# Kernel tuning notes

Measured on AMD Instinct MI355X. Metric: run time of the kernel, lower is better.

The kernel has to match this reference:

```python
import jax, jax.numpy as jnp
import numpy as np
import math

E = 512
H = 2048
P = 128  # attention_limit

def _make_params(key):
    ks = jax.random.split(key, 6)
    s = 0.02
    p = {}
    p['wq'] = jax.random.normal(ks[0], (E, E), jnp.float32) * s
    p['bq'] = jnp.zeros((E,), jnp.float32)
    p['wk'] = jax.random.normal(ks[1], (E, E), jnp.float32) * s
    p['bk'] = jnp.zeros((E,), jnp.float32)
    p['wv'] = jax.random.normal(ks[2], (E, E), jnp.float32) * s
    p['bv'] = jnp.zeros((E,), jnp.float32)
    p['w1'] = jax.random.normal(ks[3], (E, H), jnp.float32) * s
    p['b1'] = jnp.zeros((H,), jnp.float32)
    p['w2'] = jax.random.normal(ks[4], (H, E), jnp.float32) * s
    p['b2'] = jnp.zeros((E,), jnp.float32)
    p['ln1_w'] = jnp.ones((E,), jnp.float32)
    p['ln1_b'] = jnp.zeros((E,), jnp.float32)
    p['ln2_w'] = jnp.ones((E,), jnp.float32)
    p['ln2_b'] = jnp.zeros((E,), jnp.float32)
    return p

def setup_inputs() -> dict:
    key = jax.random.key(0)
    kx, kp = jax.random.split(key)
    inp = {'x': jax.random.normal(kx, (2, 1024, E), jnp.float32)}
    inp.update(_make_params(kp))
    return inp

def _layernorm(x, w, b, eps=1e-5):
    mu = jnp.mean(x, axis=-1, keepdims=True)
    var = jnp.mean((x - mu) ** 2, axis=-1, keepdims=True)
    return (x - mu) / jnp.sqrt(var + eps) * w + b

def _forward(x, wq, bq, wk, bk, wv, bv, w1, b1, w2, b2, ln1_w, ln1_b, ln2_w, ln2_b):
    B, S, Ed = x.shape
    # "RoPE" is actually additive sinusoidal PE in the source
    pos = jnp.arange(S, dtype=jnp.float32)[:, None]
    div = jnp.exp(jnp.arange(0, Ed, 2, dtype=jnp.float32) * (-math.log(10000.0) / Ed))
    pe = jnp.zeros((S, Ed), jnp.float32)
    pe = pe.at[:, 0::2].set(jnp.sin(pos * div))
    pe = pe.at[:, 1::2].set(jnp.cos(pos * div))
    x = x + pe[None]

    # local attention: pad x first, then apply K/V linears (padded rows -> bias)
    x_ext = jnp.pad(x, ((0, 0), (P, P), (0, 0)))
    q = x @ wq + bq                      # [B,S,E]
    k_ext = x_ext @ wk + bk              # [B,S+2P,E]
    v_ext = x_ext @ wv + bv
    W = 2 * P + 1
    win_idx = jnp.arange(S)[:, None] + jnp.arange(W)[None, :]  # [S,W]
    k_win = k_ext[:, win_idx]            # [B,S,W,E]
    v_win = v_ext[:, win_idx]            # [B,S,W,E]
    energy = jnp.einsum('bse,bswe->bsw', q, k_win) / jnp.sqrt(jnp.float32(Ed))
    attn = jax.nn.softmax(energy, axis=-1)
    attn_out = jnp.einsum('bsw,bswe->bse', attn, v_win)

    x = _layernorm(attn_out + x, ln1_w, ln1_b)
    ff = jnp.maximum(x @ w1 + b1, 0.0) @ w2 + b2
    return _layernorm(ff + x, ln2_w, ln2_b)

def reference(x, wq, bq, wk, bk, wv, bv, w1, b1, w2, b2, ln1_w, ln1_b, ln2_w, ln2_b):
    return _forward(x, wq, bq, wk, bk, wv, bv, w1, b1, w2, b2, ln1_w, ln1_b, ln2_w, ln2_b)
```

## Files before the change

kernel.cpp:

```cpp
#include <hip/hip_runtime.h>
#include <hip/hip_bf16.h>

#define S_LEN 1024
#define E_DIM 512
#define H_DIM 2048
#define EXTA 1296
#define BS_ROWS 2048

typedef __attribute__((ext_vector_type(8))) short bf16x8;
typedef __attribute__((ext_vector_type(4))) float f32x4;

__device__ inline ushort f2bf(float x) {
  union { float f; unsigned u; } c; c.f = x;
  unsigned u = c.u;
  u += 0x7fffu + ((u >> 16) & 1u);
  return (ushort)(u >> 16);
}
__device__ inline float bf2f(ushort u) {
  union { unsigned u; float f; } c;
  c.u = ((unsigned)u) << 16;
  return c.f;
}

__device__ inline void gload16(ushort* dst, const ushort* src) {
  __builtin_amdgcn_global_load_lds(
      (const __attribute__((address_space(1))) void*)src,
      (__attribute__((address_space(3))) void*)dst, 16, 0, 0);
}

__global__ __launch_bounds__(256) void prep_kernel(const float* __restrict__ x,
                                                   const float* __restrict__ wq,
                                                   const float* __restrict__ wk,
                                                   const float* __restrict__ wv,
                                                   ushort* __restrict__ xpe_bf,
                                                   ushort* __restrict__ wqkvT) {
  __shared__ float t[32][33];
  const int blk = blockIdx.x;
  if (blk < 2048) {
    int idx = blk * 256 + threadIdx.x;
    int e = idx & (E_DIM - 1);
    int s = idx >> 9;
    const float c = -9.210340371976184f / 512.0f;
    float freq = expf((float)(e & ~1) * c);
    float ang = (float)s * freq;
    float pe = (e & 1) ? cosf(ang) : sinf(ang);
    xpe_bf[idx] = f2bf(x[idx] + pe);
    xpe_bf[idx + S_LEN * E_DIM] = f2bf(x[idx + S_LEN * E_DIM] + pe);
  } else {
    const int tile = blk - 2048;
    const int sect = tile >> 8, tt = tile & 255;
    const float* W = sect == 0 ? wq : (sect == 1 ? wk : wv);
    ushort* WT = wqkvT + (size_t)sect * 512 * 512;
    const int bx = tt & 15, by = tt >> 4;
    int lx = threadIdx.x & 31, ly = threadIdx.x >> 5;
    int n0 = bx * 32, k0 = by * 32;
#pragma unroll
    for (int r = 0; r < 4; ++r)
      t[ly + r * 8][lx] = W[(size_t)(k0 + ly + r * 8) * 512 + n0 + lx];
    __syncthreads();
#pragma unroll
    for (int r = 0; r < 4; ++r)
      WT[(size_t)(n0 + ly + r * 8) * 512 + k0 + lx] = f2bf(t[lx][ly + r * 8]);
  }
}

__global__ __launch_bounds__(256) void qkv_pad_kernel(const ushort* __restrict__ A,
                                                      const ushort* __restrict__ Bt,
                                                      const float* __restrict__ bq,
                                                      const float* __restrict__ bk,
                                                      const float* __restrict__ bv,
                                                      ushort* __restrict__ q_out,
                                                      ushort* __restrict__ k_out,
                                                      ushort* __restrict__ v_out) {
  __shared__ ushort As[64 * 64];
  __shared__ ushort Bs[128 * 64];
  const int blk = blockIdx.x;
  const int tid = threadIdx.x;

  if (blk >= 384) {
    int p = (blk - 384) * 256 + tid;
    int t2 = p / (2 * 272 * 512);
    int r2 = p % (2 * 272 * 512);
    int b = r2 / (272 * 512);
    int r3 = r2 % (272 * 512);
    if (t2 == 0) {
      int rr = r3 >> 9, e = r3 & 511;
      int row = rr < 128 ? rr : 1024 + rr;
      float v = rr < 256 ? bk[e] : 0.f;
      k_out[((size_t)b * EXTA + row) * 512 + e] = f2bf(v);
    } else {
      int n = r3 / 272, jj = r3 % 272;
      int j = jj < 128 ? jj : 1024 + jj;
      float v = jj < 256 ? bv[n] : 0.f;
      v_out[((size_t)b * 512 + n) * EXTA + j] = f2bf(v);
    }
    return;
  }

  const int lane = tid & 63;
  const int w = tid >> 6;
  const int wr = w >> 1, wc = w & 1;
  const int l15 = lane & 15, lhi = lane >> 4;
  const int col0 = (blk % 12) * 128, row0 = (blk / 12) * 64;

  f32x4 acc[2][4] = {};

  for (int k0 = 0; k0 < 512; k0 += 64) {
#pragma unroll
    for (int it = 0; it < 2; ++it) {
      int u = it * 256 + tid;
      int r = u >> 3;
      int c16 = (u & 7) ^ (r & 7);
      gload16(&As[(size_t)u * 8], &A[(size_t)(row0 + r) * 512 + k0 + c16 * 8]);
    }
#pragma unroll
    for (int it = 0; it < 4; ++it) {
      int u = it * 256 + tid;
      int r = u >> 3;
      int c16 = (u & 7) ^ (r & 7);
      gload16(&Bs[(size_t)u * 8], &Bt[(size_t)(col0 + r) * 512 + k0 + c16 * 8]);
    }
    __syncthreads();
#pragma unroll
    for (int kk = 0; kk < 2; ++kk) {
      bf16x8 af[2], bfr[4];
#pragma unroll
      for (int mi = 0; mi < 2; ++mi) {
        int r = wr * 32 + mi * 16 + l15;
        int c16 = (kk * 4 + lhi) ^ (r & 7);
        af[mi] = *(const bf16x8*)&As[r * 64 + c16 * 8];
      }
#pragma unroll
      for (int ni = 0; ni < 4; ++ni) {
        int r = wc * 64 + ni * 16 + l15;
        int c16 = (kk * 4 + lhi) ^ (r & 7);
        bfr[ni] = *(const bf16x8*)&Bs[r * 64 + c16 * 8];
      }
#pragma unroll
      for (int mi = 0; mi < 2; ++mi)
#pragma unroll
        for (int ni = 0; ni < 4; ++ni)
          acc[mi][ni] = __builtin_amdgcn_mfma_f32_16x16x32_bf16(af[mi], bfr[ni], acc[mi][ni], 0, 0, 0);
    }
    __syncthreads();
  }

#pragma unroll
  for (int mi = 0; mi < 2; ++mi) {
    int mbase = row0 + wr * 32 + mi * 16 + lhi * 4;
#pragma unroll
    for (int ni = 0; ni < 4; ++ni) {
      int n = col0 + wc * 64 + ni * 16 + l15;
      int sect = n >> 9, nn = n & 511;
      float b = sect == 0 ? bq[nn] : (sect == 1 ? bk[nn] : bv[nn]);
      int bb = mbase >> 10;
      int s = mbase & 1023;
      if (sect == 0) {
#pragma unroll
        for (int j = 0; j < 4; ++j)
          q_out[(size_t)(mbase + j) * 512 + nn] = f2bf(acc[mi][ni][j] + b);
      } else if (sect == 1) {
#pragma unroll
        for (int j = 0; j < 4; ++j)
          k_out[((size_t)bb * EXTA + 128 + s + j) * 512 + nn] = f2bf(acc[mi][ni][j] + b);
      } else {
        ushort4 pk;
        pk.x = f2bf(acc[mi][ni][0] + b);
        pk.y = f2bf(acc[mi][ni][1] + b);
        pk.z = f2bf(acc[mi][ni][2] + b);
        pk.w = f2bf(acc[mi][ni][3] + b);
        *(ushort4*)&v_out[((size_t)bb * 512 + nn) * EXTA + 128 + s] = pk;
      }
    }
  }
}

template <int BM, int BN, int WM, int WN, int OUT>
__global__ __launch_bounds__(256) void mfma_gemm(const ushort* __restrict__ A,
                                                 const ushort* __restrict__ Bt,
                                                 const float* __restrict__ bias,
                                                 void* __restrict__ Cout,
                                                 int M, int N, int K, int LDA) {
  constexpr int WAVES_N = BN / WN;
  constexpr int FM = WM / 16, FN = WN / 16;
  __shared__ ushort As[BM * 64];
  __shared__ ushort Bs[BN * 64];
  const int tid = threadIdx.x;
  const int lane = tid & 63;
  const int w = tid >> 6;
  const int wr = w / WAVES_N, wc = w % WAVES_N;
  const int l15 = lane & 15, lhi = lane >> 4;
  const int col0 = blockIdx.x * BN, row0 = blockIdx.y * BM;
  const int koff = blockIdx.z * K;

  f32x4 acc[FM][FN] = {};

  for (int k0 = 0; k0 < K; k0 += 64) {
#pragma unroll
    for (int it = 0; it < BM / 32; ++it) {
      int u = it * 256 + tid;
      int r = u >> 3;
      int c16 = (u & 7) ^ (r & 7);
      gload16(&As[(size_t)u * 8], &A[(size_t)(row0 + r) * LDA + koff + k0 + c16 * 8]);
    }
#pragma unroll
    for (int it = 0; it < BN / 32; ++it) {
      int u = it * 256 + tid;
      int r = u >> 3;
      int c16 = (u & 7) ^ (r & 7);
      gload16(&Bs[(size_t)u * 8], &Bt[(size_t)(col0 + r) * LDA + koff + k0 + c16 * 8]);
    }
    __syncthreads();
#pragma unroll
    for (int kk = 0; kk < 2; ++kk) {
      bf16x8 af[FM], bfr[FN];
#pragma unroll
      for (int mi = 0; mi < FM; ++mi) {
        int r = wr * WM + mi * 16 + l15;
        int c16 = (kk * 4 + lhi) ^ (r & 7);
        af[mi] = *(const bf16x8*)&As[r * 64 + c16 * 8];
      }
#pragma unroll
      for (int ni = 0; ni < FN; ++ni) {
        int r = wc * WN + ni * 16 + l15;
        int c16 = (kk * 4 + lhi) ^ (r & 7);
        bfr[ni] = *(const bf16x8*)&Bs[r * 64 + c16 * 8];
      }
#pragma unroll
      for (int mi = 0; mi < FM; ++mi)
#pragma unroll
        for (int ni = 0; ni < FN; ++ni)
          acc[mi][ni] = __builtin_amdgcn_mfma_f32_16x16x32_bf16(af[mi], bfr[ni], acc[mi][ni], 0, 0, 0);
    }
    __syncthreads();
  }

#pragma unroll
  for (int mi = 0; mi < FM; ++mi) {
    int mbase = row0 + wr * WM + mi * 16 + lhi * 4;
#pragma unroll
    for (int ni = 0; ni < FN; ++ni) {
      int n = col0 + wc * WN + ni * 16 + l15;
      if constexpr (OUT == 1) {
        float b = bias[n];
        ushort* C = (ushort*)Cout;
#pragma unroll
        for (int j = 0; j < 4; ++j)
          C[(size_t)(mbase + j) * N + n] = f2bf(fmaxf(acc[mi][ni][j] + b, 0.f));
      } else {
        float* C = (float*)Cout + (size_t)blockIdx.z * M * N;
#pragma unroll
        for (int j = 0; j < 4; ++j) C[(size_t)(mbase + j) * N + n] = acc[mi][ni][j];
      }
    }
  }
}

union AttnSm {
  struct {
    float e[16][292];
    ushort p[16][296];
    float inv[16];
    float redS[8][16];
    float redQ[8][16];
    float mu[16], rs[16];
  } a;
  float t[32][33];
};

__global__ __launch_bounds__(512) void attn_ln1(const ushort* __restrict__ qb,
                                                const ushort* __restrict__ kb,
                                                const ushort* __restrict__ vt,
                                                const ushort* __restrict__ xpe_bf,
                                                const float* __restrict__ ln1w,
                                                const float* __restrict__ ln1b,
                                                const float* __restrict__ w1,
                                                const float* __restrict__ w2,
                                                ushort* __restrict__ w1T,
                                                ushort* __restrict__ w2T,
                                                ushort* __restrict__ x1bf) {
  __shared__ AttnSm sm;
  const int tid = threadIdx.x;

  if (blockIdx.x >= 128) {
    const int tile = blockIdx.x - 128;
    const float* W; ushort* WT; int K, N, bx, by;
    if (tile < 1024) {
      K = 512; N = 2048; W = w1; WT = w1T;
      bx = tile & 63; by = tile >> 6;
    } else {
      K = 2048; N = 512; W = w2; WT = w2T;
      int tt = tile - 1024; bx = tt & 15; by = tt >> 4;
    }
    int lx = tid & 31, ly = tid >> 5;
    int n0 = bx * 32, k0 = by * 32;
#pragma unroll
    for (int r = 0; r < 2; ++r)
      sm.t[ly + r * 16][lx] = W[(size_t)(k0 + ly + r * 16) * N + n0 + lx];
    __syncthreads();
#pragma unroll
    for (int r = 0; r < 2; ++r)
      WT[(size_t)(n0 + ly + r * 16) * K + k0 + lx] = f2bf(sm.t[lx][ly + r * 16]);
    return;
  }

  const int lane = tid & 63;
  const int w = tid >> 6;
  const int l15 = lane & 15, lhi = lane >> 4;
  const int tile = blockIdx.x;
  const int b = tile >> 6;
  const int s0 = (tile & 63) * 16;
  const int base0 = b * 1024 + s0;

  const ushort* qrow = qb + (size_t)(base0 + l15) * 512 + lhi * 8;
  bf16x8 qf[16];
#pragma unroll
  for (int ks = 0; ks < 16; ++ks) qf[ks] = *(const bf16x8*)(qrow + ks * 32);

  const float scale = 0.044194173824159216f;
  const ushort* kbase = kb + (size_t)b * EXTA * 512 + (size_t)(s0 + l15) * 512 + lhi * 8;

  for (int jt = w; jt < 18; jt += 8) {
    f32x4 acc = {};
    const ushort* kp = kbase + (size_t)jt * 16 * 512;
#pragma unroll
    for (int ks = 0; ks < 16; ++ks) {
      bf16x8 kf = *(const bf16x8*)(kp + ks * 32);
      acc = __builtin_amdgcn_mfma_f32_16x16x32_bf16(qf[ks], kf, acc, 0, 0, 0);
    }
    int jc = jt * 16 + l15;
#pragma unroll
    for (int j = 0; j < 4; ++j) {
      int i = lhi * 4 + j;
      bool valid = (jc >= i) && (jc <= i + 256);
      sm.a.e[i][jc] = valid ? acc[j] * scale : -1e30f;
    }
  }
  __syncthreads();

  {
    int r = tid >> 5, c0 = tid & 31;
    float m = -1e30f;
#pragma unroll
    for (int t = 0; t < 9; ++t) m = fmaxf(m, sm.a.e[r][c0 + 32 * t]);
#pragma unroll
    for (int off = 1; off <= 16; off <<= 1) m = fmaxf(m, __shfl_xor(m, off));
    float s = 0.f;
#pragma unroll
    for (int t = 0; t < 9; ++t) {
      float p = __expf(sm.a.e[r][c0 + 32 * t] - m);
      s += p;
      sm.a.p[r][c0 + 32 * t] = f2bf(p);
    }
#pragma unroll
    for (int off = 1; off <= 16; off <<= 1) s += __shfl_xor(s, off);
    if (c0 == 0) sm.a.inv[r] = 1.0f / s;
  }
  __syncthreads();

  bf16x8 pf[9];
#pragma unroll
  for (int ks = 0; ks < 9; ++ks) pf[ks] = *(const bf16x8*)&sm.a.p[l15][ks * 32 + lhi * 8];
  float inv[4];
#pragma unroll
  for (int j = 0; j < 4; ++j) inv[j] = sm.a.inv[lhi * 4 + j];

  const ushort* vbase = vt + (size_t)b * 512 * EXTA + s0 + lhi * 8;
  float val[4][4];
#pragma unroll
  for (int ni = 0; ni < 4; ++ni) {
    int n = w * 64 + ni * 16 + l15;
    f32x4 acc = {};
    const ushort* vp = vbase + (size_t)n * EXTA;
#pragma unroll
    for (int ks = 0; ks < 9; ++ks) {
      bf16x8 vf = *(const bf16x8*)(vp + ks * 32);
      acc = __builtin_amdgcn_mfma_f32_16x16x32_bf16(pf[ks], vf, acc, 0, 0, 0);
    }
#pragma unroll
    for (int j = 0; j < 4; ++j) {
      int r = lhi * 4 + j;
      val[ni][j] = acc[j] * inv[j] + bf2f(xpe_bf[(size_t)(base0 + r) * 512 + n]);
    }
  }

  float S[4], Q[4];
#pragma unroll
  for (int j = 0; j < 4; ++j) {
    S[j] = 0.f; Q[j] = 0.f;
#pragma unroll
    for (int ni = 0; ni < 4; ++ni) { S[j] += val[ni][j]; Q[j] += val[ni][j] * val[ni][j]; }
  }
#pragma unroll
  for (int off = 1; off <= 8; off <<= 1) {
#pragma unroll
    for (int j = 0; j < 4; ++j) {
      S[j] += __shfl_xor(S[j], off);
      Q[j] += __shfl_xor(Q[j], off);
    }
  }
  if (l15 == 0) {
#pragma unroll
    for (int j = 0; j < 4; ++j) { sm.a.redS[w][lhi * 4 + j] = S[j]; sm.a.redQ[w][lhi * 4 + j] = Q[j]; }
  }
  __syncthreads();
  if (tid < 16) {
    float sS = 0.f, sQ = 0.f;
#pragma unroll
    for (int ww = 0; ww < 8; ++ww) { sS += sm.a.redS[ww][tid]; sQ += sm.a.redQ[ww][tid]; }
    float mu = sS * (1.0f / 512.0f);
    float var = sQ * (1.0f / 512.0f) - mu * mu;
    sm.a.mu[tid] = mu;
    sm.a.rs[tid] = rsqrtf(var + 1e-5f);
  }
  __syncthreads();

#pragma unroll
  for (int ni = 0; ni < 4; ++ni) {
    int n = w * 64 + ni * 16 + l15;
    float lw = ln1w[n], lb = ln1b[n];
#pragma unroll
    for (int j = 0; j < 4; ++j) {
      int r = lhi * 4 + j;
      float o = (val[ni][j] - sm.a.mu[r]) * sm.a.rs[r] * lw + lb;
      x1bf[(size_t)(base0 + r) * 512 + n] = f2bf(o);
    }
  }
}

__device__ inline float wave_reduce_sum(float v) {
#pragma unroll
  for (int off = 32; off >= 1; off >>= 1) v += __shfl_xor(v, off);
  return v;
}

__global__ __launch_bounds__(256) void ln2_kernel(const float* __restrict__ parts,
                                                  const float* __restrict__ ab,
                                                  const ushort* __restrict__ rsd_bf,
                                                  const float* __restrict__ w,
                                                  const float* __restrict__ bias,
                                                  float* __restrict__ out) {
  const int row = blockIdx.x;
  const int tid = threadIdx.x;
  __shared__ float red[8];
  const int e0 = tid * 2;
  const size_t base = (size_t)row * E_DIM + e0;
  const size_t PART = (size_t)BS_ROWS * E_DIM;
  float2 v0 = *(const float2*)(parts + base);
  float2 v1 = *(const float2*)(parts + PART + base);
  float2 bb = *(const float2*)(ab + e0);
  ushort2 rv = *(const ushort2*)(rsd_bf + base);
  float x0 = v0.x + v1.x + bb.x + bf2f(rv.x);
  float x1 = v0.y + v1.y + bb.y + bf2f(rv.y);

  float sm = wave_reduce_sum(x0 + x1);
  if ((tid & 63) == 0) red[tid >> 6] = sm;
  __syncthreads();
  float mu = (red[0] + red[1] + red[2] + red[3]) * (1.0f / 512.0f);
  float d0 = x0 - mu, d1 = x1 - mu;
  float vs = wave_reduce_sum(d0 * d0 + d1 * d1);
  if ((tid & 63) == 0) red[4 + (tid >> 6)] = vs;
  __syncthreads();
  float var = (red[4] + red[5] + red[6] + red[7]) * (1.0f / 512.0f);
  float inv = rsqrtf(var + 1e-5f);
  float2 wv = *(const float2*)(w + e0);
  float2 bi = *(const float2*)(bias + e0);
  float o0 = d0 * inv * wv.x + bi.x;
  float o1 = d1 * inv * wv.y + bi.y;
  *(float2*)(out + base) = make_float2(o0, o1);
}

extern "C" void kernel_launch(void* const* d_in, const int* in_sizes, int n_in,
                              void* d_out, int out_size, void* d_ws, size_t ws_size,
                              hipStream_t stream) {
  const float* x    = (const float*)d_in[0];
  const float* wq   = (const float*)d_in[1];
  const float* bq   = (const float*)d_in[2];
  const float* wk   = (const float*)d_in[3];
  const float* bk   = (const float*)d_in[4];
  const float* wv   = (const float*)d_in[5];
  const float* bv   = (const float*)d_in[6];
  const float* w1   = (const float*)d_in[7];
  const float* b1   = (const float*)d_in[8];
  const float* w2   = (const float*)d_in[9];
  const float* b2   = (const float*)d_in[10];
  const float* ln1w = (const float*)d_in[11];
  const float* ln1b = (const float*)d_in[12];
  const float* ln2w = (const float*)d_in[13];
  const float* ln2b = (const float*)d_in[14];

  char* W = (char*)d_ws;
  ushort* xpebf  = (ushort*)(W);
  ushort* wqkvT  = (ushort*)(W + (2u  << 20));
  ushort* w1T    = (ushort*)(W + (4u  << 20));
  ushort* w2T    = (ushort*)(W + (6u  << 20));
  ushort* q_bf   = (ushort*)(W + (8u  << 20));
  ushort* k_bf   = (ushort*)(W + (10u << 20));
  ushort* v_t    = (ushort*)(W + (13u << 20));
  ushort* x1bf   = (ushort*)(W + (16u << 20));
  ushort* ff1_bf = (ushort*)(W + (18u << 20));
  float*  ff2    = (float*)(W + (26u << 20));

  prep_kernel<<<2816, 256, 0, stream>>>(x, wq, wk, wv, xpebf, wqkvT);

  qkv_pad_kernel<<<2560, 256, 0, stream>>>(xpebf, wqkvT, bq, bk, bv, q_bf, k_bf, v_t);

  attn_ln1<<<2176, 512, 0, stream>>>(q_bf, k_bf, v_t, xpebf, ln1w, ln1b,
                                     w1, w2, w1T, w2T, x1bf);

  mfma_gemm<64, 128, 32, 64, 1><<<dim3(16, 32), 256, 0, stream>>>(
      x1bf, w1T, b1, ff1_bf, BS_ROWS, H_DIM, 512, 512);

  mfma_gemm<64, 64, 32, 32, 3><<<dim3(8, 32, 2), 256, 0, stream>>>(
      ff1_bf, w2T, nullptr, ff2, BS_ROWS, E_DIM, 1024, 2048);

  ln2_kernel<<<BS_ROWS, 256, 0, stream>>>(ff2, b2, x1bf, ln2w, ln2b, (float*)d_out);
}
```

Baseline: 72.39 us.

## Shrink QKV tiles, widen attention blocks to 1024 threads, vectorize PE prep

The positional-encoding prep now handles two adjacent elements per thread, computing one sincos and using float2/ushort2 accesses, which halves that part of the grid. The QKV GEMM tile shrinks from 64x128 to 64x64, doubling the block count so more CUs get work. The attention+LN1 kernel moves to 1024 threads (16 waves), with each wave owning one softmax row and 32 output columns. The trade-offs are less data reuse per QKV tile and higher register and occupancy pressure from the larger attention blocks.

```diff
diff --git a/kernel.cpp b/kernel.cpp
--- a/kernel.cpp
+++ b/kernel.cpp
@@ -36,18 +36,25 @@
                                                    ushort* __restrict__ wqkvT) {
   __shared__ float t[32][33];
   const int blk = blockIdx.x;
-  if (blk < 2048) {
+  if (blk < 1024) {
     int idx = blk * 256 + threadIdx.x;
-    int e = idx & (E_DIM - 1);
-    int s = idx >> 9;
+    int ep = idx & 255;
+    int s = idx >> 8;
+    int e0 = ep * 2;
     const float c = -9.210340371976184f / 512.0f;
-    float freq = expf((float)(e & ~1) * c);
-    float ang = (float)s * freq;
-    float pe = (e & 1) ? cosf(ang) : sinf(ang);
-    xpe_bf[idx] = f2bf(x[idx] + pe);
-    xpe_bf[idx + S_LEN * E_DIM] = f2bf(x[idx + S_LEN * E_DIM] + pe);
+    float freq = __expf((float)e0 * c);
+    float sn, cs;
+    __sincosf((float)s * freq, &sn, &cs);
+    size_t base = (size_t)s * E_DIM + e0;
+    float2 x0 = *(const float2*)(x + base);
+    float2 x1 = *(const float2*)(x + base + S_LEN * E_DIM);
+    ushort2 o0, o1;
+    o0.x = f2bf(x0.x + sn); o0.y = f2bf(x0.y + cs);
+    o1.x = f2bf(x1.x + sn); o1.y = f2bf(x1.y + cs);
+    *(ushort2*)(xpe_bf + base) = o0;
+    *(ushort2*)(xpe_bf + base + S_LEN * E_DIM) = o1;
   } else {
-    const int tile = blk - 2048;
+    const int tile = blk - 1024;
     const int sect = tile >> 8, tt = tile & 255;
     const float* W = sect == 0 ? wq : (sect == 1 ? wk : wv);
     ushort* WT = wqkvT + (size_t)sect * 512 * 512;
@@ -73,12 +80,12 @@
                                                       ushort* __restrict__ k_out,
                                                       ushort* __restrict__ v_out) {
   __shared__ ushort As[64 * 64];
-  __shared__ ushort Bs[128 * 64];
+  __shared__ ushort Bs[64 * 64];
   const int blk = blockIdx.x;
   const int tid = threadIdx.x;
 
-  if (blk >= 384) {
-    int p = (blk - 384) * 256 + tid;
+  if (blk >= 768) {
+    int p = (blk - 768) * 256 + tid;
     int t2 = p / (2 * 272 * 512);
     int r2 = p % (2 * 272 * 512);
     int b = r2 / (272 * 512);
@@ -101,9 +108,9 @@
   const int w = tid >> 6;
   const int wr = w >> 1, wc = w & 1;
   const int l15 = lane & 15, lhi = lane >> 4;
-  const int col0 = (blk % 12) * 128, row0 = (blk / 12) * 64;
-
-  f32x4 acc[2][4] = {};
+  const int col0 = (blk % 24) * 64, row0 = (blk / 24) * 64;
+
+  f32x4 acc[2][2] = {};
 
   for (int k0 = 0; k0 < 512; k0 += 64) {
 #pragma unroll
@@ -114,7 +121,7 @@
       gload16(&As[(size_t)u * 8], &A[(size_t)(row0 + r) * 512 + k0 + c16 * 8]);
     }
 #pragma unroll
-    for (int it = 0; it < 4; ++it) {
+    for (int it = 0; it < 2; ++it) {
       int u = it * 256 + tid;
       int r = u >> 3;
       int c16 = (u & 7) ^ (r & 7);
@@ -123,7 +130,7 @@
     __syncthreads();
 #pragma unroll
     for (int kk = 0; kk < 2; ++kk) {
-      bf16x8 af[2], bfr[4];
+      bf16x8 af[2], bfr[2];
 #pragma unroll
       for (int mi = 0; mi < 2; ++mi) {
         int r = wr * 32 + mi * 16 + l15;
@@ -131,15 +138,15 @@
         af[mi] = *(const bf16x8*)&As[r * 64 + c16 * 8];
       }
 #pragma unroll
-      for (int ni = 0; ni < 4; ++ni) {
-        int r = wc * 64 + ni * 16 + l15;
+      for (int ni = 0; ni < 2; ++ni) {
+        int r = wc * 32 + ni * 16 + l15;
         int c16 = (kk * 4 + lhi) ^ (r & 7);
         bfr[ni] = *(const bf16x8*)&Bs[r * 64 + c16 * 8];
       }
 #pragma unroll
       for (int mi = 0; mi < 2; ++mi)
 #pragma unroll
-        for (int ni = 0; ni < 4; ++ni)
+        for (int ni = 0; ni < 2; ++ni)
           acc[mi][ni] = __builtin_amdgcn_mfma_f32_16x16x32_bf16(af[mi], bfr[ni], acc[mi][ni], 0, 0, 0);
     }
     __syncthreads();
@@ -149,8 +156,8 @@
   for (int mi = 0; mi < 2; ++mi) {
     int mbase = row0 + wr * 32 + mi * 16 + lhi * 4;
 #pragma unroll
-    for (int ni = 0; ni < 4; ++ni) {
-      int n = col0 + wc * 64 + ni * 16 + l15;
+    for (int ni = 0; ni < 2; ++ni) {
+      int n = col0 + wc * 32 + ni * 16 + l15;
       int sect = n >> 9, nn = n & 511;
       float b = sect == 0 ? bq[nn] : (sect == 1 ? bk[nn] : bv[nn]);
       int bb = mbase >> 10;
@@ -261,24 +268,24 @@
     float e[16][292];
     ushort p[16][296];
     float inv[16];
-    float redS[8][16];
-    float redQ[8][16];
+    float redS[16][16];
+    float redQ[16][16];
     float mu[16], rs[16];
   } a;
   float t[32][33];
 };
 
-__global__ __launch_bounds__(512) void attn_ln1(const ushort* __restrict__ qb,
-                                                const ushort* __restrict__ kb,
-                                                const ushort* __restrict__ vt,
-                                                const ushort* __restrict__ xpe_bf,
-                                                const float* __restrict__ ln1w,
-                                                const float* __restrict__ ln1b,
-                                                const float* __restrict__ w1,
-                                                const float* __restrict__ w2,
-                                                ushort* __restrict__ w1T,
-                                                ushort* __restrict__ w2T,
-                                                ushort* __restrict__ x1bf) {
+__global__ __launch_bounds__(1024) void attn_ln1(const ushort* __restrict__ qb,
+                                                 const ushort* __restrict__ kb,
+                                                 const ushort* __restrict__ vt,
+                                                 const ushort* __restrict__ xpe_bf,
+                                                 const float* __restrict__ ln1w,
+                                                 const float* __restrict__ ln1b,
+                                                 const float* __restrict__ w1,
+                                                 const float* __restrict__ w2,
+                                                 ushort* __restrict__ w1T,
+                                                 ushort* __restrict__ w2T,
+                                                 ushort* __restrict__ x1bf) {
   __shared__ AttnSm sm;
   const int tid = threadIdx.x;
 
@@ -294,13 +301,9 @@
     }
     int lx = tid & 31, ly = tid >> 5;
     int n0 = bx * 32, k0 = by * 32;
-#pragma unroll
-    for (int r = 0; r < 2; ++r)
-      sm.t[ly + r * 16][lx] = W[(size_t)(k0 + ly + r * 16) * N + n0 + lx];
+    sm.t[ly][lx] = W[(size_t)(k0 + ly) * N + n0 + lx];
     __syncthreads();
-#pragma unroll
-    for (int r = 0; r < 2; ++r)
-      WT[(size_t)(n0 + ly + r * 16) * K + k0 + lx] = f2bf(sm.t[lx][ly + r * 16]);
+    WT[(size_t)(n0 + ly) * K + k0 + lx] = f2bf(sm.t[lx][ly]);
     return;
   }
 
@@ -320,7 +323,7 @@
   const float scale = 0.044194173824159216f;
   const ushort* kbase = kb + (size_t)b * EXTA * 512 + (size_t)(s0 + l15) * 512 + lhi * 8;
 
-  for (int jt = w; jt < 18; jt += 8) {
+  for (int jt = w; jt < 18; jt += 16) {
     f32x4 acc = {};
     const ushort* kp = kbase + (size_t)jt * 16 * 512;
 #pragma unroll
@@ -339,22 +342,29 @@
   __syncthreads();
 
   {
-    int r = tid >> 5, c0 = tid & 31;
+    int r = w;
     float m = -1e30f;
 #pragma unroll
-    for (int t = 0; t < 9; ++t) m = fmaxf(m, sm.a.e[r][c0 + 32 * t]);
-#pragma unroll
-    for (int off = 1; off <= 16; off <<= 1) m = fmaxf(m, __shfl_xor(m, off));
+    for (int t = 0; t < 5; ++t) {
+      int col = lane + 64 * t;
+      float e = (t < 4 || lane < 32) ? sm.a.e[r][col] : -1e30f;
+      m = fmaxf(m, e);
+    }
+#pragma unroll
+    for (int off = 1; off <= 32; off <<= 1) m = fmaxf(m, __shfl_xor(m, off));
     float s = 0.f;
 #pragma unroll
-    for (int t = 0; t < 9; ++t) {
-      float p = __expf(sm.a.e[r][c0 + 32 * t] - m);
-      s += p;
-      sm.a.p[r][c0 + 32 * t] = f2bf(p);
-    }
-#pragma unroll
-    for (int off = 1; off <= 16; off <<= 1) s += __shfl_xor(s, off);
-    if (c0 == 0) sm.a.inv[r] = 1.0f / s;
+    for (int t = 0; t < 5; ++t) {
+      int col = lane + 64 * t;
+      if (t < 4 || lane < 32) {
+        float p = __expf(sm.a.e[r][col] - m);
+        s += p;
+        sm.a.p[r][col] = f2bf(p);
+      }
+    }
+#pragma unroll
+    for (int off = 1; off <= 32; off <<= 1) s += __shfl_xor(s, off);
+    if (lane == 0) sm.a.inv[r] = 1.0f / s;
   }
   __syncthreads();
 
@@ -366,10 +376,10 @@
   for (int j = 0; j < 4; ++j) inv[j] = sm.a.inv[lhi * 4 + j];
 
   const ushort* vbase = vt + (size_t)b * 512 * EXTA + s0 + lhi * 8;
-  float val[4][4];
-#pragma unroll
-  for (int ni = 0; ni < 4; ++ni) {
-    int n = w * 64 + ni * 16 + l15;
+  float val[2][4];
+#pragma unroll
+  for (int ni = 0; ni < 2; ++ni) {
+    int n = w * 32 + ni * 16 + l15;
     f32x4 acc = {};
     const ushort* vp = vbase + (size_t)n * EXTA;
 #pragma unroll
@@ -389,7 +399,7 @@
   for (int j = 0; j < 4; ++j) {
     S[j] = 0.f; Q[j] = 0.f;
 #pragma unroll
-    for (int ni = 0; ni < 4; ++ni) { S[j] += val[ni][j]; Q[j] += val[ni][j] * val[ni][j]; }
+    for (int ni = 0; ni < 2; ++ni) { S[j] += val[ni][j]; Q[j] += val[ni][j] * val[ni][j]; }
   }
 #pragma unroll
   for (int off = 1; off <= 8; off <<= 1) {
@@ -407,7 +417,7 @@
   if (tid < 16) {
     float sS = 0.f, sQ = 0.f;
 #pragma unroll
-    for (int ww = 0; ww < 8; ++ww) { sS += sm.a.redS[ww][tid]; sQ += sm.a.redQ[ww][tid]; }
+    for (int ww = 0; ww < 16; ++ww) { sS += sm.a.redS[ww][tid]; sQ += sm.a.redQ[ww][tid]; }
     float mu = sS * (1.0f / 512.0f);
     float var = sQ * (1.0f / 512.0f) - mu * mu;
     sm.a.mu[tid] = mu;
@@ -416,8 +426,8 @@
   __syncthreads();
 
 #pragma unroll
-  for (int ni = 0; ni < 4; ++ni) {
-    int n = w * 64 + ni * 16 + l15;
+  for (int ni = 0; ni < 2; ++ni) {
+    int n = w * 32 + ni * 16 + l15;
     float lw = ln1w[n], lb = ln1b[n];
 #pragma unroll
     for (int j = 0; j < 4; ++j) {
@@ -501,12 +511,12 @@
   ushort* ff1_bf = (ushort*)(W + (18u << 20));
   float*  ff2    = (float*)(W + (26u << 20));
 
-  prep_kernel<<<2816, 256, 0, stream>>>(x, wq, wk, wv, xpebf, wqkvT);
-
-  qkv_pad_kernel<<<2560, 256, 0, stream>>>(xpebf, wqkvT, bq, bk, bv, q_bf, k_bf, v_t);
-
-  attn_ln1<<<2176, 512, 0, stream>>>(q_bf, k_bf, v_t, xpebf, ln1w, ln1b,
-                                     w1, w2, w1T, w2T, x1bf);
+  prep_kernel<<<1792, 256, 0, stream>>>(x, wq, wk, wv, xpebf, wqkvT);
+
+  qkv_pad_kernel<<<2944, 256, 0, stream>>>(xpebf, wqkvT, bq, bk, bv, q_bf, k_bf, v_t);
+
+  attn_ln1<<<2176, 1024, 0, stream>>>(q_bf, k_bf, v_t, xpebf, ln1w, ln1b,
+                                      w1, w2, w1T, w2T, x1bf);
 
   mfma_gemm<64, 128, 32, 64, 1><<<dim3(16, 32), 256, 0, stream>>>(
       x1bf, w1T, b1, ff1_bf, BS_ROWS, H_DIM, 512, 512);
```

Measured after the change: 72.08 us. Within noise of the previous version (-0.4%).
